# Optimization experiments

Hardware: AMD Instinct MI355X
Metric: run time of the kernel (lower is better)

Reference implementation:

```python
import jax, jax.numpy as jnp
import numpy as np

N = 50000      # nodes
E = 800000     # edges (before self-loops)
H = 2          # attention heads
C = 64         # hidden_channels (per-head out since concat=False)
L = 3          # num_layers - 2 conv blocks
OUT = 128      # readout out_channels
G = 512        # num graphs
VOCAB = 100    # embedding table size
NEG_SLOPE = 0.2


def setup_inputs() -> dict:
    key = jax.random.key(0)
    ks = jax.random.split(key, 12)
    s = 1.0 / np.sqrt(C)
    x = jax.random.randint(ks[0], (N,), 0, VOCAB, dtype=jnp.int32)
    edge_index = jax.random.randint(ks[1], (2, E), 0, N, dtype=jnp.int32)
    batch = jnp.sort(jax.random.randint(ks[2], (N,), 0, G, dtype=jnp.int32))
    embed = jax.random.normal(ks[3], (VOCAB, C), dtype=jnp.float32) * s
    lin_W = jax.random.normal(ks[4], (L, C, C), dtype=jnp.float32) * s
    lin_b = jnp.zeros((L, C), dtype=jnp.float32)
    gat_Wl = jax.random.normal(ks[5], (L, C, H * C), dtype=jnp.float32) * s
    gat_bl = jnp.zeros((L, H * C), dtype=jnp.float32)
    gat_Wr = jax.random.normal(ks[6], (L, C, H * C), dtype=jnp.float32) * s
    gat_br = jnp.zeros((L, H * C), dtype=jnp.float32)
    gat_att = jax.random.normal(ks[7], (L, H, C), dtype=jnp.float32) * s
    gat_bias = jnp.zeros((L, C), dtype=jnp.float32)
    readout_W = jax.random.normal(ks[8], (C, OUT), dtype=jnp.float32) * s
    readout_b = jnp.zeros((OUT,), dtype=jnp.float32)
    return {"x": x, "edge_index": edge_index, "batch": batch, "num_graphs": G,
            "embed": embed, "lin_W": lin_W, "lin_b": lin_b,
            "gat_Wl": gat_Wl, "gat_bl": gat_bl, "gat_Wr": gat_Wr, "gat_br": gat_br,
            "gat_att": gat_att, "gat_bias": gat_bias,
            "readout_W": readout_W, "readout_b": readout_b}


def _gatv2_layer(h, src, dst, Wl, bl, Wr, br, att, bias):
    # lin_l -> source/message features, lin_r -> target features (PyG GATv2Conv)
    xl = (h @ Wl + bl).reshape(N, H, C)
    xr = (h @ Wr + br).reshape(N, H, C)
    # per-edge GATv2 score: a^T LeakyReLU(x_l[j] + x_r[i])
    e = jax.nn.leaky_relu(xl[src] + xr[dst], NEG_SLOPE)      # [E2,H,C]
    score = jnp.einsum('ehc,hc->eh', e, att)                 # [E2,H]
    # segment softmax over incoming edges of each dst node (stable)
    m = jax.lax.stop_gradient(jax.ops.segment_max(score, dst, num_segments=N))
    p = jnp.exp(score - m[dst])
    denom = jax.ops.segment_sum(p, dst, num_segments=N)      # [N,H]
    alpha = p / denom[dst]                                   # [E2,H]
    msg = xl[src] * alpha[:, :, None]                        # [E2,H,C]
    agg = jax.ops.segment_sum(msg, dst, num_segments=N)      # [N,H,C]
    return agg.mean(axis=1) + bias                           # concat=False -> head mean


def reference(x, edge_index, batch, num_graphs, embed, lin_W, lin_b,
              gat_Wl, gat_bl, gat_Wr, gat_br, gat_att, gat_bias,
              readout_W, readout_b):
    # add self loops (GATv2Conv default add_self_loops=True)
    loops = jnp.arange(N, dtype=edge_index.dtype)
    src = jnp.concatenate([edge_index[0], loops])
    dst = jnp.concatenate([edge_index[1], loops])
    h = embed[x]                                             # [N,C]
    for l in range(L):
        h = jax.nn.relu(h @ lin_W[l] + lin_b[l])             # dropout is a no-op in eval
        h = _gatv2_layer(h, src, dst, gat_Wl[l], gat_bl[l], gat_Wr[l], gat_br[l],
                         gat_att[l], gat_bias[l])
    out = h @ readout_W + readout_b                          # [N,OUT]
    return jax.ops.segment_sum(out, batch, num_segments=num_graphs)  # [G,OUT]
```

## Files before the change

### kernel.cpp

```cpp
#include <hip/hip_runtime.h>
#include <hip/hip_fp16.h>

#define N_NODES  50000
#define E_EDGES  800000
#define E_TOT    850000
#define H_HEADS  2
#define C_DIM    64
#define HC       128
#define L_LAYERS 3
#define OUT_DIM  128
#define G_GRAPHS 512
#define NEG_SLOPE 0.2f
#define SCAN_B   196
#define NB       196
#define EPB      4096

typedef float v2f __attribute__((ext_vector_type(2)));

__device__ __forceinline__ void lds_fence() { asm volatile("" ::: "memory"); }

__global__ void embed_kernel(const int* __restrict__ x, const float* __restrict__ embed,
                             float* __restrict__ h, int* __restrict__ counts) {
    int i = blockIdx.x * 256 + threadIdx.x;
    if (i < N_NODES) counts[i] = 0;
    if (i >= N_NODES * C_DIM) return;
    int n = i >> 6, c = i & 63;
    h[i] = embed[x[n] * C_DIM + c];
}

__global__ void csr_count_kernel(const int* __restrict__ dsts, int* __restrict__ counts) {
    int e = blockIdx.x * 256 + threadIdx.x;
    if (e >= E_TOT) return;
    int d = (e < E_EDGES) ? dsts[e] : e - E_EDGES;
    atomicAdd(&counts[d], 1);
}

__global__ void scan_partial_kernel(const int* __restrict__ counts, int* __restrict__ row_ptr,
                                    int* __restrict__ partials) {
    __shared__ int wsum[4];
    int i = blockIdx.x * 256 + threadIdx.x;
    int lane = threadIdx.x & 63, wid = threadIdx.x >> 6;
    int cnt = (i < N_NODES) ? counts[i] : 0;
    int v = cnt;
#pragma unroll
    for (int off = 1; off < 64; off <<= 1) {
        int t = __shfl_up(v, off, 64);
        if (lane >= off) v += t;
    }
    if (lane == 63) wsum[wid] = v;
    __syncthreads();
    int woff = 0;
#pragma unroll
    for (int w = 0; w < 4; w++) if (w < wid) woff += wsum[w];
    v += woff;
    if (i < N_NODES) row_ptr[i] = v - cnt;
    if (threadIdx.x == 255) partials[blockIdx.x] = v;
}

__global__ void scan_offsets_kernel(const int* __restrict__ partials, int* __restrict__ block_off) {
    __shared__ int wsum[4];
    int tid = threadIdx.x;
    int lane = tid & 63, wid = tid >> 6;
    int cnt = (tid < SCAN_B) ? partials[tid] : 0;
    int v = cnt;
#pragma unroll
    for (int off = 1; off < 64; off <<= 1) {
        int t = __shfl_up(v, off, 64);
        if (lane >= off) v += t;
    }
    if (lane == 63) wsum[wid] = v;
    __syncthreads();
    int woff = 0;
#pragma unroll
    for (int w = 0; w < 4; w++) if (w < wid) woff += wsum[w];
    v += woff;
    if (tid < SCAN_B) block_off[tid] = v - cnt;
}

__global__ void scan_add_kernel(int* __restrict__ row_ptr, const int* __restrict__ block_off,
                                int* __restrict__ bwptr) {
    int i = blockIdx.x * 256 + threadIdx.x;
    if (i < N_NODES) {
        int v = row_ptr[i] + block_off[blockIdx.x];
        row_ptr[i] = v;
        if ((i & 255) == 0) bwptr[i >> 8] = v;
    }
    if (i == 0) row_ptr[N_NODES] = E_TOT;
}

__global__ void edge_partition_kernel(const int* __restrict__ srcs, const int* __restrict__ dsts,
                                      int* __restrict__ bwptr, unsigned int* __restrict__ ebuf) {
    __shared__ int hist[256];
    __shared__ int lscan[256];
    __shared__ int sExcl[256];
    __shared__ int lcnt[256];
    __shared__ int gbase[256];
    __shared__ unsigned int sval[EPB];
    __shared__ unsigned char sgid[EPB];
    int tid = threadIdx.x;
    int ebase = blockIdx.x * EPB;
    hist[tid] = 0;
    __syncthreads();
    unsigned int val[16];
    int gid[16];
#pragma unroll
    for (int i = 0; i < 16; i++) {
        int e = ebase + i * 256 + tid;
        if (e < E_TOT) {
            int s, d;
            if (e < E_EDGES) { s = srcs[e]; d = dsts[e]; }
            else             { s = d = e - E_EDGES; }
            val[i] = ((unsigned)s << 8) | (unsigned)(d & 255);
            gid[i] = d >> 8;
            atomicAdd(&hist[gid[i]], 1);
        } else gid[i] = -1;
    }
    __syncthreads();
    lscan[tid] = hist[tid];
    __syncthreads();
#pragma unroll
    for (int off = 1; off < 256; off <<= 1) {
        int t = (tid >= off) ? lscan[tid - off] : 0;
        __syncthreads();
        lscan[tid] += t;
        __syncthreads();
    }
    sExcl[tid] = lscan[tid] - hist[tid];
    lcnt[tid] = 0;
    __syncthreads();
#pragma unroll
    for (int i = 0; i < 16; i++) {
        if (gid[i] >= 0) {
            int off = atomicAdd(&lcnt[gid[i]], 1);
            int idx = sExcl[gid[i]] + off;
            sval[idx] = val[i];
            sgid[idx] = (unsigned char)gid[i];
        }
    }
    if (tid < NB) {
        int c = hist[tid];
        gbase[tid] = c ? atomicAdd(&bwptr[tid], c) : 0;
    }
    __syncthreads();
    int total = lscan[255];
    for (int idx = tid; idx < total; idx += 256) {
        int g = sgid[idx];
        ebuf[gbase[g] + (idx - sExcl[g])] = sval[idx];
    }
}

__global__ void bucket_csr_kernel(const unsigned int* __restrict__ ebuf,
                                  const int* __restrict__ row_ptr,
                                  unsigned short* __restrict__ src_sorted) {
    __shared__ int lbase[256];
    __shared__ int lcnt[256];
    int g = blockIdx.x, tid = threadIdx.x;
    int n0 = g << 8;
    int nodes = min(256, N_NODES - n0);
    int b0 = row_ptr[n0];
    int b1 = row_ptr[min(n0 + 256, N_NODES)];
    if (tid < nodes) lbase[tid] = row_ptr[n0 + tid] - b0;
    lcnt[tid] = 0;
    __syncthreads();
    int cnt = b1 - b0;
    for (int i = tid; i < cnt; i += 256) {
        unsigned int v = ebuf[b0 + i];
        int dl = v & 255;
        int slot = lbase[dl] + atomicAdd(&lcnt[dl], 1);
        src_sorted[b0 + slot] = (unsigned short)(v >> 8);
    }
}

__global__ void layer_lin_kernel(const float* __restrict__ h,
                                 const float* __restrict__ W, const float* __restrict__ b,
                                 const float* __restrict__ Wl, const float* __restrict__ bl,
                                 const float* __restrict__ Wr, const float* __restrict__ br,
                                 __half* __restrict__ xlh, float* __restrict__ xri) {
    __shared__ float sH[16 * 64];
    __shared__ float sH2[16 * 64];
    int tid = threadIdx.x;
    int base = blockIdx.x * 16;
#pragma unroll
    for (int i = 0; i < 4; i++) {
        int idx = tid + i * 256;
        int nn = base + (idx >> 6);
        sH[idx] = (nn < N_NODES) ? h[(size_t)nn * 64 + (idx & 63)] : 0.f;
    }
    __syncthreads();
    {
        int c = tid & 63, g = tid >> 6;
        float a0 = b[c], a1 = a0, a2 = a0, a3 = a0;
        for (int k = 0; k < 64; k++) {
            float wv = W[k * 64 + c];
            a0 = fmaf(sH[(g * 4 + 0) * 64 + k], wv, a0);
            a1 = fmaf(sH[(g * 4 + 1) * 64 + k], wv, a1);
            a2 = fmaf(sH[(g * 4 + 2) * 64 + k], wv, a2);
            a3 = fmaf(sH[(g * 4 + 3) * 64 + k], wv, a3);
        }
        sH2[(g * 4 + 0) * 64 + c] = fmaxf(a0, 0.f);
        sH2[(g * 4 + 1) * 64 + c] = fmaxf(a1, 0.f);
        sH2[(g * 4 + 2) * 64 + c] = fmaxf(a2, 0.f);
        sH2[(g * 4 + 3) * 64 + c] = fmaxf(a3, 0.f);
    }
    __syncthreads();
    {
        int j = tid & 127, gg = tid >> 7;
        float accl[8], accr[8];
#pragma unroll
        for (int n = 0; n < 8; n++) { accl[n] = bl[j]; accr[n] = br[j]; }
        for (int k = 0; k < 64; k++) {
            float wl = Wl[k * 128 + j], wr = Wr[k * 128 + j];
#pragma unroll
            for (int n = 0; n < 8; n++) {
                float hv = sH2[(gg * 8 + n) * 64 + k];
                accl[n] = fmaf(hv, wl, accl[n]);
                accr[n] = fmaf(hv, wr, accr[n]);
            }
        }
        int hh = j >> 6, c = j & 63;
#pragma unroll
        for (int n = 0; n < 8; n++) {
            int node = base + gg * 8 + n;
            if (node < N_NODES) {
                size_t o = (size_t)node * 128 + c * 2 + hh;
                xlh[o] = __float2half(accl[n]);
                xri[o] = accr[n];
            }
        }
    }
}

__global__ void gat_kernel(const __half2* __restrict__ xlh, const float2* __restrict__ xr2,
                           const float* __restrict__ att, const int* __restrict__ row_ptr,
                           const unsigned short* __restrict__ src_sorted,
                           const float* __restrict__ bias,
                           float* __restrict__ h_out) {
    __shared__ __align__(16) float cbuf[4][8 * 132];
    int w = threadIdx.x >> 6;
    int d = blockIdx.x * 4 + w;
    if (d >= N_NODES) return;
    int lane = threadIdx.x & 63;
    int r0 = row_ptr[d], r1 = row_ptr[d + 1];
    float2 vrf = xr2[(size_t)d * 64 + lane];
    v2f vr2 = {vrf.x, vrf.y};
    v2f att2 = {att[lane], att[64 + lane]};
    float* cb = cbuf[w];
    int e_of = lane >> 3, p = lane & 7;

    float dpx = 0.f, dpy = 0.f;
    v2f ac0 = {0.f, 0.f}, ac1 = {0.f, 0.f};

#define GAT_LOAD(V, CB) do {                                                    \
        int lim_ = nchunk - 1;                                                  \
        _Pragma("unroll")                                                       \
        for (int e = 0; e < 8; e++) {                                           \
            int ee_ = (CB) + e;                                                 \
            int sv_ = __builtin_amdgcn_readlane(idx, (ee_ < nchunk) ? ee_ : lim_); \
            V[e] = xlh[(size_t)sv_ * 64 + lane];                                \
        }                                                                       \
    } while (0)

#define GAT_PROC(V, CB) do {                                                    \
        int rem_ = nchunk - (CB);                                               \
        v2f vf8[8];                                                             \
        _Pragma("unroll")                                                       \
        for (int e = 0; e < 8; e++) {                                           \
            float2 vf_ = __half22float2(V[e]);                                  \
            v2f vl2 = {vf_.x, vf_.y};                                           \
            vf8[e] = vl2;                                                       \
            v2f z = vl2 + vr2;                                                  \
            v2f t = __builtin_elementwise_max(z, z * NEG_SLOPE) * att2;         \
            *(v2f*)&cb[e * 132 + 2 * lane] = t;                                 \
        }                                                                       \
        lds_fence();                                                            \
        v2f s2 = {0.f, 0.f};                                                    \
        {                                                                       \
            const float4* row_ = (const float4*)&cb[e_of * 132 + p * 16];       \
            _Pragma("unroll")                                                   \
            for (int j = 0; j < 4; j++) {                                       \
                float4 f = row_[j];                                             \
                s2 += (v2f){f.x, f.y};                                          \
                s2 += (v2f){f.z, f.w};                                          \
            }                                                                   \
        }                                                                       \
        lds_fence();                                                            \
        _Pragma("unroll")                                                       \
        for (int off = 1; off <= 4; off <<= 1) {                                \
            v2f o_;                                                             \
            o_.x = __shfl_xor(s2.x, off, 64);                                   \
            o_.y = __shfl_xor(s2.y, off, 64);                                   \
            s2 += o_;                                                           \
        }                                                                       \
        float sx = s2.x, sy = s2.y;                                             \
        if (e_of >= rem_) { sx = -INFINITY; sy = -INFINITY; }                   \
        float wx = __expf(sx), wy = __expf(sy);                                 \
        dpx += wx; dpy += wy;                                                   \
        _Pragma("unroll")                                                       \
        for (int e = 0; e < 8; e++) {                                           \
            float swx = __int_as_float(__builtin_amdgcn_readlane(__float_as_int(wx), 8 * e)); \
            float swy = __int_as_float(__builtin_amdgcn_readlane(__float_as_int(wy), 8 * e)); \
            v2f w2 = {swx, swy};                                                \
            if (e & 1) ac1 = __builtin_elementwise_fma(w2, vf8[e], ac1);        \
            else       ac0 = __builtin_elementwise_fma(w2, vf8[e], ac0);        \
        }                                                                       \
    } while (0)

    for (int base = r0; base < r1; base += 64) {
        int a = base + lane;
        int idx = (int)src_sorted[(a < r1) ? a : (r1 - 1)];
        int nchunk = min(64, r1 - base);
        __half2 va[8], vb[8];
        GAT_LOAD(va, 0);
        int cb_i = 0;
        for (;;) {
            int nx = cb_i + 8;
            if (nx < nchunk) {
                GAT_LOAD(vb, nx);
                GAT_PROC(va, cb_i);
                cb_i = nx;
            } else {
                GAT_PROC(va, cb_i);
                break;
            }
            nx = cb_i + 8;
            if (nx < nchunk) {
                GAT_LOAD(va, nx);
                GAT_PROC(vb, cb_i);
                cb_i = nx;
            } else {
                GAT_PROC(vb, cb_i);
                break;
            }
        }
    }
#undef GAT_LOAD
#undef GAT_PROC

#pragma unroll
    for (int off = 8; off <= 32; off <<= 1) {
        dpx += __shfl_xor(dpx, off, 64);
        dpy += __shfl_xor(dpy, off, 64);
    }
    v2f acc = ac0 + ac1;
    h_out[(size_t)d * 64 + lane] = (acc.x / dpx + acc.y / dpy) * 0.5f + bias[lane];
}

__global__ void zero_out_kernel(float* __restrict__ out) {
    int i = blockIdx.x * 256 + threadIdx.x;
    if (i < G_GRAPHS * OUT_DIM) out[i] = 0.f;
}

__global__ void readout_kernel(const float* __restrict__ h, const float* __restrict__ W,
                               const float* __restrict__ b, const int* __restrict__ batch,
                               float* __restrict__ out) {
    __shared__ float sH[16 * 64];
    __shared__ int sB[16];
    int tid = threadIdx.x;
    int base = blockIdx.x * 16;
#pragma unroll
    for (int i = 0; i < 4; i++) {
        int idx = tid + i * 256;
        int nn = base + (idx >> 6);
        sH[idx] = (nn < N_NODES) ? h[(size_t)nn * 64 + (idx & 63)] : 0.f;
    }
    if (tid < 16) sB[tid] = (base + tid < N_NODES) ? batch[base + tid] : -1;
    __syncthreads();
    int j = tid & 127, gg = tid >> 7;
    float acc[8];
#pragma unroll
    for (int n = 0; n < 8; n++) acc[n] = b[j];
    for (int k = 0; k < 64; k++) {
        float wv = W[k * OUT_DIM + j];
#pragma unroll
        for (int n = 0; n < 8; n++) acc[n] = fmaf(sH[(gg * 8 + n) * 64 + k], wv, acc[n]);
    }
    float run = 0.f; int curb = -2;
#pragma unroll
    for (int n = 0; n < 8; n++) {
        int node = base + gg * 8 + n;
        int bb = (node < N_NODES) ? sB[gg * 8 + n] : -1;
        if (bb != curb) {
            if (curb >= 0) atomicAdd(&out[curb * OUT_DIM + j], run);
            run = 0.f; curb = bb;
        }
        if (bb >= 0) run += acc[n];
    }
    if (curb >= 0) atomicAdd(&out[curb * OUT_DIM + j], run);
}

extern "C" void kernel_launch(void* const* d_in, const int* in_sizes, int n_in,
                              void* d_out, int out_size, void* d_ws, size_t ws_size,
                              hipStream_t stream) {
    const int*   x        = (const int*)d_in[0];
    const int*   edge     = (const int*)d_in[1];
    const int*   batch    = (const int*)d_in[2];
    const float* embed    = (const float*)d_in[4];
    const float* lin_W    = (const float*)d_in[5];
    const float* lin_b    = (const float*)d_in[6];
    const float* gat_Wl   = (const float*)d_in[7];
    const float* gat_bl   = (const float*)d_in[8];
    const float* gat_Wr   = (const float*)d_in[9];
    const float* gat_br   = (const float*)d_in[10];
    const float* gat_att  = (const float*)d_in[11];
    const float* gat_bias = (const float*)d_in[12];
    const float* ro_W     = (const float*)d_in[13];
    const float* ro_b     = (const float*)d_in[14];
    float* out = (float*)d_out;

    const int* srcs = edge;
    const int* dsts = edge + E_EDGES;

    float* h    = (float*)d_ws;
    __half* xlh = (__half*)(h + (size_t)N_NODES * 64);
    float* xr   = (float*)((char*)xlh + (size_t)N_NODES * HC * sizeof(__half));
    int* counts     = (int*)(xr + (size_t)N_NODES * HC);
    int* row_ptr    = counts + N_NODES;
    int* bwptr      = row_ptr + N_NODES + 1;
    int* partials   = bwptr + 256;
    int* block_off  = partials + SCAN_B;
    unsigned int* ebuf = (unsigned int*)(block_off + SCAN_B);
    unsigned short* src_sorted = (unsigned short*)(ebuf + E_TOT);

    const int T = 256;
    const int gEmbed = (N_NODES * C_DIM + 255) / 256;
    const int gEdge  = (E_TOT + 255) / 256;
    const int gPart  = (E_TOT + EPB - 1) / EPB;
    const int gLin   = (N_NODES + 15) / 16;
    const int gGat   = (N_NODES + 3) / 4;
    const int gOut   = (G_GRAPHS * OUT_DIM + 255) / 256;

    embed_kernel<<<gEmbed, T, 0, stream>>>(x, embed, h, counts);

    csr_count_kernel<<<gEdge, T, 0, stream>>>(dsts, counts);
    scan_partial_kernel<<<SCAN_B, T, 0, stream>>>(counts, row_ptr, partials);
    scan_offsets_kernel<<<1, T, 0, stream>>>(partials, block_off);
    scan_add_kernel<<<SCAN_B, T, 0, stream>>>(row_ptr, block_off, bwptr);
    edge_partition_kernel<<<gPart, T, 0, stream>>>(srcs, dsts, bwptr, ebuf);
    bucket_csr_kernel<<<NB, T, 0, stream>>>(ebuf, row_ptr, src_sorted);

    for (int l = 0; l < L_LAYERS; l++) {
        layer_lin_kernel<<<gLin, T, 0, stream>>>(
            h,
            lin_W + (size_t)l * 64 * 64, lin_b + (size_t)l * 64,
            gat_Wl + (size_t)l * 64 * 128, gat_bl + (size_t)l * 128,
            gat_Wr + (size_t)l * 64 * 128, gat_br + (size_t)l * 128,
            xlh, xr);
        gat_kernel<<<gGat, T, 0, stream>>>(
            (const __half2*)xlh, (const float2*)xr, gat_att + (size_t)l * HC,
            row_ptr, src_sorted, gat_bias + (size_t)l * 64, h);
    }

    zero_out_kernel<<<gOut, T, 0, stream>>>(out);
    readout_kernel<<<gLin, T, 0, stream>>>(h, ro_W, ro_b, batch, out);
}
```

Measured before the change: 451.9 us.

## Rebuild CSR via bucket histograms, fuse embedding lookup, restructure GAT edge processing

```diff
diff --git a/kernel.cpp b/kernel.cpp
--- a/kernel.cpp
+++ b/kernel.cpp
@@ -11,36 +11,41 @@
 #define OUT_DIM  128
 #define G_GRAPHS 512
 #define NEG_SLOPE 0.2f
-#define SCAN_B   196
 #define NB       196
 #define EPB      4096
 
 typedef float v2f __attribute__((ext_vector_type(2)));
 
-__device__ __forceinline__ void lds_fence() { asm volatile("" ::: "memory"); }
-
-__global__ void embed_kernel(const int* __restrict__ x, const float* __restrict__ embed,
-                             float* __restrict__ h, int* __restrict__ counts) {
+__global__ void init_kernel(float* __restrict__ out, int* __restrict__ bucket_counts) {
     int i = blockIdx.x * 256 + threadIdx.x;
-    if (i < N_NODES) counts[i] = 0;
-    if (i >= N_NODES * C_DIM) return;
-    int n = i >> 6, c = i & 63;
-    h[i] = embed[x[n] * C_DIM + c];
-}
-
-__global__ void csr_count_kernel(const int* __restrict__ dsts, int* __restrict__ counts) {
-    int e = blockIdx.x * 256 + threadIdx.x;
-    if (e >= E_TOT) return;
-    int d = (e < E_EDGES) ? dsts[e] : e - E_EDGES;
-    atomicAdd(&counts[d], 1);
-}
-
-__global__ void scan_partial_kernel(const int* __restrict__ counts, int* __restrict__ row_ptr,
-                                    int* __restrict__ partials) {
+    if (i < G_GRAPHS * OUT_DIM) out[i] = 0.f;
+    if (blockIdx.x == 0) bucket_counts[threadIdx.x] = 0;
+}
+
+__global__ void bucket_count_kernel(const int* __restrict__ dsts, int* __restrict__ bucket_counts) {
+    __shared__ int hist[256];
+    int tid = threadIdx.x;
+    hist[tid] = 0;
+    __syncthreads();
+    int ebase = blockIdx.x * EPB;
+#pragma unroll
+    for (int i = 0; i < 16; i++) {
+        int e = ebase + i * 256 + tid;
+        if (e < E_TOT) {
+            int d = (e < E_EDGES) ? dsts[e] : e - E_EDGES;
+            atomicAdd(&hist[d >> 8], 1);
+        }
+    }
+    __syncthreads();
+    if (hist[tid]) atomicAdd(&bucket_counts[tid], hist[tid]);
+}
+
+__global__ void scan196_kernel(const int* __restrict__ bucket_counts,
+                               int* __restrict__ bwptr, int* __restrict__ bbase) {
     __shared__ int wsum[4];
-    int i = blockIdx.x * 256 + threadIdx.x;
-    int lane = threadIdx.x & 63, wid = threadIdx.x >> 6;
-    int cnt = (i < N_NODES) ? counts[i] : 0;
+    int tid = threadIdx.x;
+    int lane = tid & 63, wid = tid >> 6;
+    int cnt = (tid < NB) ? bucket_counts[tid] : 0;
     int v = cnt;
 #pragma unroll
     for (int off = 1; off < 64; off <<= 1) {
@@ -53,39 +58,8 @@
 #pragma unroll
     for (int w = 0; w < 4; w++) if (w < wid) woff += wsum[w];
     v += woff;
-    if (i < N_NODES) row_ptr[i] = v - cnt;
-    if (threadIdx.x == 255) partials[blockIdx.x] = v;
-}
-
-__global__ void scan_offsets_kernel(const int* __restrict__ partials, int* __restrict__ block_off) {
-    __shared__ int wsum[4];
-    int tid = threadIdx.x;
-    int lane = tid & 63, wid = tid >> 6;
-    int cnt = (tid < SCAN_B) ? partials[tid] : 0;
-    int v = cnt;
-#pragma unroll
-    for (int off = 1; off < 64; off <<= 1) {
-        int t = __shfl_up(v, off, 64);
-        if (lane >= off) v += t;
-    }
-    if (lane == 63) wsum[wid] = v;
-    __syncthreads();
-    int woff = 0;
-#pragma unroll
-    for (int w = 0; w < 4; w++) if (w < wid) woff += wsum[w];
-    v += woff;
-    if (tid < SCAN_B) block_off[tid] = v - cnt;
-}
-
-__global__ void scan_add_kernel(int* __restrict__ row_ptr, const int* __restrict__ block_off,
-                                int* __restrict__ bwptr) {
-    int i = blockIdx.x * 256 + threadIdx.x;
-    if (i < N_NODES) {
-        int v = row_ptr[i] + block_off[blockIdx.x];
-        row_ptr[i] = v;
-        if ((i & 255) == 0) bwptr[i >> 8] = v;
-    }
-    if (i == 0) row_ptr[N_NODES] = E_TOT;
+    if (tid < NB) { bwptr[tid] = v - cnt; bbase[tid] = v - cnt; }
+    if (tid == 0) bbase[NB] = E_TOT;
 }
 
 __global__ void edge_partition_kernel(const int* __restrict__ srcs, const int* __restrict__ dsts,
@@ -150,28 +124,53 @@
 }
 
 __global__ void bucket_csr_kernel(const unsigned int* __restrict__ ebuf,
-                                  const int* __restrict__ row_ptr,
+                                  const int* __restrict__ bbase,
+                                  int* __restrict__ row_ptr,
                                   unsigned short* __restrict__ src_sorted) {
-    __shared__ int lbase[256];
+    __shared__ int hist[256];
     __shared__ int lcnt[256];
+    __shared__ int wsum[4];
     int g = blockIdx.x, tid = threadIdx.x;
     int n0 = g << 8;
     int nodes = min(256, N_NODES - n0);
-    int b0 = row_ptr[n0];
-    int b1 = row_ptr[min(n0 + 256, N_NODES)];
-    if (tid < nodes) lbase[tid] = row_ptr[n0 + tid] - b0;
+    int b0 = bbase[g], b1 = bbase[g + 1];
+    int cnt = b1 - b0;
+    hist[tid] = 0;
     lcnt[tid] = 0;
     __syncthreads();
-    int cnt = b1 - b0;
+    for (int i = tid; i < cnt; i += 256) atomicAdd(&hist[ebuf[b0 + i] & 255], 1);
+    __syncthreads();
+    int c = hist[tid];
+    int v = c;
+    int lane = tid & 63, wid = tid >> 6;
+#pragma unroll
+    for (int off = 1; off < 64; off <<= 1) {
+        int t = __shfl_up(v, off, 64);
+        if (lane >= off) v += t;
+    }
+    if (lane == 63) wsum[wid] = v;
+    __syncthreads();
+    int woff = 0;
+#pragma unroll
+    for (int w = 0; w < 4; w++) if (w < wid) woff += wsum[w];
+    v += woff;
+    int nbase = b0 + v - c;
+    if (tid < nodes) row_ptr[n0 + tid] = nbase;
+    if (g == NB - 1 && tid == 0) row_ptr[N_NODES] = E_TOT;
+    __syncthreads();
+    hist[tid] = nbase;
+    __syncthreads();
     for (int i = tid; i < cnt; i += 256) {
-        unsigned int v = ebuf[b0 + i];
-        int dl = v & 255;
-        int slot = lbase[dl] + atomicAdd(&lcnt[dl], 1);
-        src_sorted[b0 + slot] = (unsigned short)(v >> 8);
+        unsigned int e = ebuf[b0 + i];
+        int dl = e & 255;
+        int slot = hist[dl] + atomicAdd(&lcnt[dl], 1);
+        src_sorted[slot] = (unsigned short)(e >> 8);
     }
 }
 
 __global__ void layer_lin_kernel(const float* __restrict__ h,
+                                 const int* __restrict__ xs, const float* __restrict__ etab,
+                                 int use_embed,
                                  const float* __restrict__ W, const float* __restrict__ b,
                                  const float* __restrict__ Wl, const float* __restrict__ bl,
                                  const float* __restrict__ Wr, const float* __restrict__ br,
@@ -184,7 +183,11 @@
     for (int i = 0; i < 4; i++) {
         int idx = tid + i * 256;
         int nn = base + (idx >> 6);
-        sH[idx] = (nn < N_NODES) ? h[(size_t)nn * 64 + (idx & 63)] : 0.f;
+        int cc = idx & 63;
+        float hv = 0.f;
+        if (nn < N_NODES)
+            hv = use_embed ? etab[xs[nn] * 64 + cc] : h[(size_t)nn * 64 + cc];
+        sH[idx] = hv;
     }
     __syncthreads();
     {
@@ -230,124 +233,119 @@
     }
 }
 
-__global__ void gat_kernel(const __half2* __restrict__ xlh, const float2* __restrict__ xr2,
+__global__ void gat_kernel(const uint4* __restrict__ xlh16, const float4* __restrict__ xr4,
                            const float* __restrict__ att, const int* __restrict__ row_ptr,
                            const unsigned short* __restrict__ src_sorted,
-                           const float* __restrict__ bias,
-                           float* __restrict__ h_out) {
-    __shared__ __align__(16) float cbuf[4][8 * 132];
+                           const float* __restrict__ bias, float* __restrict__ h_out) {
     int w = threadIdx.x >> 6;
     int d = blockIdx.x * 4 + w;
     if (d >= N_NODES) return;
     int lane = threadIdx.x & 63;
+    int q = lane >> 4, p = lane & 15;
     int r0 = row_ptr[d], r1 = row_ptr[d + 1];
-    float2 vrf = xr2[(size_t)d * 64 + lane];
-    v2f vr2 = {vrf.x, vrf.y};
-    v2f att2 = {att[lane], att[64 + lane]};
-    float* cb = cbuf[w];
-    int e_of = lane >> 3, p = lane & 7;
-
-    float dpx = 0.f, dpy = 0.f;
-    v2f ac0 = {0.f, 0.f}, ac1 = {0.f, 0.f};
-
-#define GAT_LOAD(V, CB) do {                                                    \
-        int lim_ = nchunk - 1;                                                  \
+
+    float4 vra = xr4[(size_t)d * 32 + 2 * p];
+    float4 vrb = xr4[(size_t)d * 32 + 2 * p + 1];
+    v2f vr2[4] = {{vra.x, vra.y}, {vra.z, vra.w}, {vrb.x, vrb.y}, {vrb.z, vrb.w}};
+    float4 ax4 = ((const float4*)att)[p];
+    float4 ay4 = ((const float4*)(att + 64))[p];
+    v2f at2[4] = {{ax4.x, ay4.x}, {ax4.y, ay4.y}, {ax4.z, ay4.z}, {ax4.w, ay4.w}};
+
+    v2f dp2 = {0.f, 0.f};
+    v2f acc2[4] = {{0.f, 0.f}, {0.f, 0.f}, {0.f, 0.f}, {0.f, 0.f}};
+
+#define GAT_LOAD(V0, V1, CB) do {                                               \
+        int c0_ = (CB) + q, c1_ = (CB) + 4 + q;                                 \
+        int s0_ = __shfl(idx, (c0_ < nchunk) ? c0_ : (nchunk - 1), 64);         \
+        int s1_ = __shfl(idx, (c1_ < nchunk) ? c1_ : (nchunk - 1), 64);         \
+        V0 = xlh16[(size_t)s0_ * 16 + p];                                       \
+        V1 = xlh16[(size_t)s1_ * 16 + p];                                       \
+    } while (0)
+
+#define GAT_SLOT(V, CE) do {                                                    \
+        const __half2* hp_ = (const __half2*)&(V);                              \
+        v2f vl2[4];                                                             \
         _Pragma("unroll")                                                       \
-        for (int e = 0; e < 8; e++) {                                           \
-            int ee_ = (CB) + e;                                                 \
-            int sv_ = __builtin_amdgcn_readlane(idx, (ee_ < nchunk) ? ee_ : lim_); \
-            V[e] = xlh[(size_t)sv_ * 64 + lane];                                \
+        for (int c = 0; c < 4; c++) {                                           \
+            float2 f_ = __half22float2(hp_[c]);                                 \
+            vl2[c] = (v2f){f_.x, f_.y};                                         \
         }                                                                       \
+        v2f t = {0.f, 0.f};                                                     \
+        _Pragma("unroll")                                                       \
+        for (int c = 0; c < 4; c++) {                                           \
+            v2f z = vl2[c] + vr2[c];                                            \
+            z = __builtin_elementwise_max(z, z * NEG_SLOPE);                    \
+            t = __builtin_elementwise_fma(z, at2[c], t);                        \
+        }                                                                       \
+        _Pragma("unroll")                                                       \
+        for (int off = 1; off <= 8; off <<= 1) {                                \
+            v2f o_;                                                             \
+            o_.x = __shfl_xor(t.x, off, 64);                                    \
+            o_.y = __shfl_xor(t.y, off, 64);                                    \
+            t += o_;                                                            \
+        }                                                                       \
+        float sx = ((CE) < nchunk) ? t.x : -INFINITY;                           \
+        float sy = ((CE) < nchunk) ? t.y : -INFINITY;                           \
+        v2f w2 = {__expf(sx), __expf(sy)};                                      \
+        dp2 += w2;                                                              \
+        _Pragma("unroll")                                                       \
+        for (int c = 0; c < 4; c++)                                             \
+            acc2[c] = __builtin_elementwise_fma(w2, vl2[c], acc2[c]);           \
     } while (0)
 
-#define GAT_PROC(V, CB) do {                                                    \
-        int rem_ = nchunk - (CB);                                               \
-        v2f vf8[8];                                                             \
-        _Pragma("unroll")                                                       \
-        for (int e = 0; e < 8; e++) {                                           \
-            float2 vf_ = __half22float2(V[e]);                                  \
-            v2f vl2 = {vf_.x, vf_.y};                                           \
-            vf8[e] = vl2;                                                       \
-            v2f z = vl2 + vr2;                                                  \
-            v2f t = __builtin_elementwise_max(z, z * NEG_SLOPE) * att2;         \
-            *(v2f*)&cb[e * 132 + 2 * lane] = t;                                 \
-        }                                                                       \
-        lds_fence();                                                            \
-        v2f s2 = {0.f, 0.f};                                                    \
-        {                                                                       \
-            const float4* row_ = (const float4*)&cb[e_of * 132 + p * 16];       \
-            _Pragma("unroll")                                                   \
-            for (int j = 0; j < 4; j++) {                                       \
-                float4 f = row_[j];                                             \
-                s2 += (v2f){f.x, f.y};                                          \
-                s2 += (v2f){f.z, f.w};                                          \
-            }                                                                   \
-        }                                                                       \
-        lds_fence();                                                            \
-        _Pragma("unroll")                                                       \
-        for (int off = 1; off <= 4; off <<= 1) {                                \
-            v2f o_;                                                             \
-            o_.x = __shfl_xor(s2.x, off, 64);                                   \
-            o_.y = __shfl_xor(s2.y, off, 64);                                   \
-            s2 += o_;                                                           \
-        }                                                                       \
-        float sx = s2.x, sy = s2.y;                                             \
-        if (e_of >= rem_) { sx = -INFINITY; sy = -INFINITY; }                   \
-        float wx = __expf(sx), wy = __expf(sy);                                 \
-        dpx += wx; dpy += wy;                                                   \
-        _Pragma("unroll")                                                       \
-        for (int e = 0; e < 8; e++) {                                           \
-            float swx = __int_as_float(__builtin_amdgcn_readlane(__float_as_int(wx), 8 * e)); \
-            float swy = __int_as_float(__builtin_amdgcn_readlane(__float_as_int(wy), 8 * e)); \
-            v2f w2 = {swx, swy};                                                \
-            if (e & 1) ac1 = __builtin_elementwise_fma(w2, vf8[e], ac1);        \
-            else       ac0 = __builtin_elementwise_fma(w2, vf8[e], ac0);        \
-        }                                                                       \
-    } while (0)
+#define GAT_PROC(V0, V1, CB) do { GAT_SLOT(V0, (CB) + q); GAT_SLOT(V1, (CB) + 4 + q); } while (0)
 
     for (int base = r0; base < r1; base += 64) {
         int a = base + lane;
         int idx = (int)src_sorted[(a < r1) ? a : (r1 - 1)];
         int nchunk = min(64, r1 - base);
-        __half2 va[8], vb[8];
-        GAT_LOAD(va, 0);
-        int cb_i = 0;
+        uint4 va0, va1, vb0, vb1;
+        GAT_LOAD(va0, va1, 0);
+        int cb = 0;
         for (;;) {
-            int nx = cb_i + 8;
+            int nx = cb + 8;
             if (nx < nchunk) {
-                GAT_LOAD(vb, nx);
-                GAT_PROC(va, cb_i);
-                cb_i = nx;
+                GAT_LOAD(vb0, vb1, nx);
+                GAT_PROC(va0, va1, cb);
+                cb = nx;
             } else {
-                GAT_PROC(va, cb_i);
+                GAT_PROC(va0, va1, cb);
                 break;
             }
-            nx = cb_i + 8;
+            nx = cb + 8;
             if (nx < nchunk) {
-                GAT_LOAD(va, nx);
-                GAT_PROC(vb, cb_i);
-                cb_i = nx;
+                GAT_LOAD(va0, va1, nx);
+                GAT_PROC(vb0, vb1, cb);
+                cb = nx;
             } else {
-                GAT_PROC(vb, cb_i);
+                GAT_PROC(vb0, vb1, cb);
                 break;
             }
         }
     }
 #undef GAT_LOAD
+#undef GAT_SLOT
 #undef GAT_PROC
 
 #pragma unroll
-    for (int off = 8; off <= 32; off <<= 1) {
-        dpx += __shfl_xor(dpx, off, 64);
-        dpy += __shfl_xor(dpy, off, 64);
-    }
-    v2f acc = ac0 + ac1;
-    h_out[(size_t)d * 64 + lane] = (acc.x / dpx + acc.y / dpy) * 0.5f + bias[lane];
-}
-
-__global__ void zero_out_kernel(float* __restrict__ out) {
-    int i = blockIdx.x * 256 + threadIdx.x;
-    if (i < G_GRAPHS * OUT_DIM) out[i] = 0.f;
+    for (int off = 16; off <= 32; off <<= 1) {
+        dp2.x += __shfl_xor(dp2.x, off, 64);
+        dp2.y += __shfl_xor(dp2.y, off, 64);
+#pragma unroll
+        for (int c = 0; c < 4; c++) {
+            acc2[c].x += __shfl_xor(acc2[c].x, off, 64);
+            acc2[c].y += __shfl_xor(acc2[c].y, off, 64);
+        }
+    }
+    if (q == 0) {
+        float4 b4 = ((const float4*)bias)[p];
+        float4 outv;
+        outv.x = (acc2[0].x / dp2.x + acc2[0].y / dp2.y) * 0.5f + b4.x;
+        outv.y = (acc2[1].x / dp2.x + acc2[1].y / dp2.y) * 0.5f + b4.y;
+        outv.z = (acc2[2].x / dp2.x + acc2[2].y / dp2.y) * 0.5f + b4.z;
+        outv.w = (acc2[3].x / dp2.x + acc2[3].y / dp2.y) * 0.5f + b4.w;
+        ((float4*)h_out)[(size_t)d * 16 + p] = outv;
+    }
 }
 
 __global__ void readout_kernel(const float* __restrict__ h, const float* __restrict__ W,
@@ -413,43 +411,36 @@
     float* h    = (float*)d_ws;
     __half* xlh = (__half*)(h + (size_t)N_NODES * 64);
     float* xr   = (float*)((char*)xlh + (size_t)N_NODES * HC * sizeof(__half));
-    int* counts     = (int*)(xr + (size_t)N_NODES * HC);
-    int* row_ptr    = counts + N_NODES;
-    int* bwptr      = row_ptr + N_NODES + 1;
-    int* partials   = bwptr + 256;
-    int* block_off  = partials + SCAN_B;
-    unsigned int* ebuf = (unsigned int*)(block_off + SCAN_B);
+    int* row_ptr       = (int*)(xr + (size_t)N_NODES * HC);
+    int* bwptr         = row_ptr + N_NODES + 1;
+    int* bbase         = bwptr + 256;
+    int* bucket_counts = bbase + 256;
+    unsigned int* ebuf = (unsigned int*)(bucket_counts + 256);
     unsigned short* src_sorted = (unsigned short*)(ebuf + E_TOT);
 
     const int T = 256;
-    const int gEmbed = (N_NODES * C_DIM + 255) / 256;
-    const int gEdge  = (E_TOT + 255) / 256;
-    const int gPart  = (E_TOT + EPB - 1) / EPB;
-    const int gLin   = (N_NODES + 15) / 16;
-    const int gGat   = (N_NODES + 3) / 4;
-    const int gOut   = (G_GRAPHS * OUT_DIM + 255) / 256;
-
-    embed_kernel<<<gEmbed, T, 0, stream>>>(x, embed, h, counts);
-
-    csr_count_kernel<<<gEdge, T, 0, stream>>>(dsts, counts);
-    scan_partial_kernel<<<SCAN_B, T, 0, stream>>>(counts, row_ptr, partials);
-    scan_offsets_kernel<<<1, T, 0, stream>>>(partials, block_off);
-    scan_add_kernel<<<SCAN_B, T, 0, stream>>>(row_ptr, block_off, bwptr);
+    const int gInit = (G_GRAPHS * OUT_DIM + 255) / 256;
+    const int gPart = (E_TOT + EPB - 1) / EPB;
+    const int gLin  = (N_NODES + 15) / 16;
+    const int gGat  = (N_NODES + 3) / 4;
+
+    init_kernel<<<gInit, T, 0, stream>>>(out, bucket_counts);
+    bucket_count_kernel<<<gPart, T, 0, stream>>>(dsts, bucket_counts);
+    scan196_kernel<<<1, T, 0, stream>>>(bucket_counts, bwptr, bbase);
     edge_partition_kernel<<<gPart, T, 0, stream>>>(srcs, dsts, bwptr, ebuf);
-    bucket_csr_kernel<<<NB, T, 0, stream>>>(ebuf, row_ptr, src_sorted);
+    bucket_csr_kernel<<<NB, T, 0, stream>>>(ebuf, bbase, row_ptr, src_sorted);
 
     for (int l = 0; l < L_LAYERS; l++) {
         layer_lin_kernel<<<gLin, T, 0, stream>>>(
-            h,
+            h, x, embed, (l == 0) ? 1 : 0,
             lin_W + (size_t)l * 64 * 64, lin_b + (size_t)l * 64,
             gat_Wl + (size_t)l * 64 * 128, gat_bl + (size_t)l * 128,
             gat_Wr + (size_t)l * 64 * 128, gat_br + (size_t)l * 128,
             xlh, xr);
         gat_kernel<<<gGat, T, 0, stream>>>(
-            (const __half2*)xlh, (const float2*)xr, gat_att + (size_t)l * HC,
+            (const uint4*)xlh, (const float4*)xr, gat_att + (size_t)l * HC,
             row_ptr, src_sorted, gat_bias + (size_t)l * 64, h);
     }
 
-    zero_out_kernel<<<gOut, T, 0, stream>>>(out);
     readout_kernel<<<gLin, T, 0, stream>>>(h, ro_W, ro_b, batch, out);
 }
```

New measurement: 427.7 us. 1.06x faster.
